# Kernel tuning notes

Measured on AMD Instinct MI355X. Metric: run time of the kernel, lower is better.

Reference implementation:

```python
import jax, jax.numpy as jnp
import numpy as np

NUM_LEVELS = 3      # init: nums_levels
SAMPLE_POINTS = 9   # init: sample_points (S+1 = 10 samples per level)


def _ste_ceil(x):
    # straight-through ceil: forward ceil(x), gradient identity
    return jnp.ceil(x) - jax.lax.stop_gradient(x) + x


def _ste_floor(x):
    return jnp.floor(x) - jax.lax.stop_gradient(x) + x


def _local_cost_volume(cv, cur_disp, radius, sample_nums):
    # cv: [B,D,H,W], cur_disp: [B,1,H,W]
    B, D, H, W = cv.shape
    lower = cur_disp - radius                                   # [B,1,H,W]
    interval = (2.0 * radius) / sample_nums                     # scalar (upper-lower)/S
    steps = jnp.arange(sample_nums + 1, dtype=cv.dtype).reshape(1, -1, 1, 1)
    cand = lower + steps * interval                             # [B,S+1,H,W]
    ceil_c = jnp.clip(_ste_ceil(cand), 0, D - 1)
    floor_c = jnp.clip(_ste_floor(cand), 0, D - 1)
    floor_rate = ceil_c - cand
    ceil_rate = 1.0 - floor_rate
    idx_c = jax.lax.stop_gradient(ceil_c).astype(jnp.int32)
    idx_f = jax.lax.stop_gradient(floor_c).astype(jnp.int32)
    vol_c = jnp.take_along_axis(cv, idx_c, axis=1)              # gather along D
    vol_f = jnp.take_along_axis(cv, idx_f, axis=1)
    return vol_c * ceil_rate + vol_f * floor_rate               # [B,S+1,H,W]


def setup_inputs() -> dict:
    key = jax.random.key(0)
    k1, k2 = jax.random.split(key)
    B, D, H, W = 16, 64, 128, 240
    cost_volume = jax.random.normal(k1, (B, D, H, W), dtype=jnp.float32)
    # current disparity estimate in [0, D-1)
    cur_disp = jax.random.uniform(k2, (B, 1, H, W), dtype=jnp.float32) * (D - 1)
    return {"cost_volume": cost_volume, "radius": 4, "cur_disp": cur_disp}


def reference(cost_volume, radius, cur_disp):
    # Build pyramid by pairwise averaging along the disparity dim
    # (equivalent to the permute + avg_pool1d(2,2) + permute in the original).
    pyramid = [cost_volume]
    cv = cost_volume
    for _ in range(NUM_LEVELS - 1):
        B, D, H, W = cv.shape
        cv = cv.reshape(B, D // 2, 2, H, W).mean(axis=2)
        pyramid.append(cv)
    outs = []
    for i in range(NUM_LEVELS):
        ref_disp = cur_disp / (2.0 ** i)
        outs.append(_local_cost_volume(pyramid[i], ref_disp, float(radius), SAMPLE_POINTS))
    return jnp.concatenate(outs, axis=1)  # [B, NUM_LEVELS*(S+1), H, W]
```

## Files before the change

kernel.cpp:

```cpp
#include <hip/hip_runtime.h>
#include <hip/hip_fp16.h>

#define BB 16
#define DD 64
#define HH 128
#define WW 240
#define HW (HH * WW)
#define NS 10
#define NL 3
#define BLK 256
#define NWORD (DD / 2)
#define GRID 512
#define NTILE (BB * HW / BLK)

__device__ inline unsigned pack2h(float lo, float hi) {
    __half2 h = __floats2half2_rn(lo, hi);
    return *reinterpret_cast<unsigned*>(&h);
}
__device__ inline float2 unpack2h(unsigned u) {
    __half2 h = *reinterpret_cast<__half2*>(&u);
    return __half22float2(h);
}
__device__ inline float exth(unsigned u, int sel) {
    unsigned short us = (unsigned short)(u >> (sel << 4));
    __half_raw hr; hr.x = us;
    return __half2float(*reinterpret_cast<__half*>(&hr));
}

__global__ __launch_bounds__(BLK) void pcv_kernel(
    const float* __restrict__ cv,
    const int* __restrict__ radius_p,
    const float* __restrict__ disp_in,
    float* __restrict__ out)
{
    __shared__ unsigned ldsw[2][NWORD * BLK];
    const int tid = threadIdx.x;
    const int bid = blockIdx.x;
    const int q  = tid & 63;
    const int jb = tid >> 6;

    const float r = (float)(*radius_p);
    const float interval = (float)((2.0 * (double)r) / 9.0);

    const int ntiles = (NTILE - bid + GRID - 1) / GRID;

    float4 rv[16];
    float  dsp;

    {
        const int t = bid;
        const int pb = t * BLK;
        const int b = pb / HW;
        const int pixbase = pb - b * HW;
        const float* src = cv + (size_t)b * DD * HW + pixbase;
        #pragma unroll
        for (int it = 0; it < 8; ++it) {
            const int j = it * 4 + jb;
            rv[2 * it]     = *reinterpret_cast<const float4*>(src + (size_t)(2 * j)     * HW + q * 4);
            rv[2 * it + 1] = *reinterpret_cast<const float4*>(src + (size_t)(2 * j + 1) * HW + q * 4);
        }
        dsp = disp_in[pb + tid];
    }

    int cur = 0;
    for (int k = 0; k < ntiles; ++k) {
        const int t = bid + k * GRID;
        const int pb = t * BLK;
        const int b = pb / HW;
        const int pix = pb - b * HW + tid;

        unsigned* buf = &ldsw[cur][0];
        #pragma unroll
        for (int it = 0; it < 8; ++it) {
            const int j = it * 4 + jb;
            uint4 wv;
            wv.x = pack2h(rv[2 * it].x, rv[2 * it + 1].x);
            wv.y = pack2h(rv[2 * it].y, rv[2 * it + 1].y);
            wv.z = pack2h(rv[2 * it].z, rv[2 * it + 1].z);
            wv.w = pack2h(rv[2 * it].w, rv[2 * it + 1].w);
            *reinterpret_cast<uint4*>(&buf[j * BLK + q * 4]) = wv;
        }
        const float disp = dsp;

        if (k + 1 < ntiles) {
            const int tn = bid + (k + 1) * GRID;
            const int pbn = tn * BLK;
            const int bn = pbn / HW;
            const int pixbase_n = pbn - bn * HW;
            const float* srcn = cv + (size_t)bn * DD * HW + pixbase_n;
            #pragma unroll
            for (int it = 0; it < 8; ++it) {
                const int j = it * 4 + jb;
                rv[2 * it]     = *reinterpret_cast<const float4*>(srcn + (size_t)(2 * j)     * HW + q * 4);
                rv[2 * it + 1] = *reinterpret_cast<const float4*>(srcn + (size_t)(2 * j + 1) * HW + q * 4);
            }
            dsp = disp_in[pbn + tid];
        }

        asm volatile("s_waitcnt lgkmcnt(0)\n\ts_barrier" ::: "memory");

        float* outp = out + (size_t)b * (NL * NS) * HW + pix;
        float rd = disp;
        int Dl = DD;
        #pragma unroll
        for (int lvl = 0; lvl < NL; ++lvl) {
            const float lower = rd - r;
            const float dmax = (float)(Dl - 1);
            #pragma unroll
            for (int s = 0; s < NS; ++s) {
                float cand = lower + (float)s * interval;
                float cc = fminf(fmaxf(ceilf(cand),  0.0f), dmax);
                float fc = fminf(fmaxf(floorf(cand), 0.0f), dmax);
                float fr = cc - cand;
                float cr = 1.0f - fr;
                int ic = (int)cc;
                int fi = (int)fc;
                float vc, vf;
                if (lvl == 0) {
                    unsigned uf = buf[(fi >> 1) * BLK + tid];
                    unsigned uc = buf[(ic >> 1) * BLK + tid];
                    vf = exth(uf, fi & 1);
                    vc = exth(uc, ic & 1);
                } else if (lvl == 1) {
                    float2 a = unpack2h(buf[fi * BLK + tid]);
                    float2 c = unpack2h(buf[ic * BLK + tid]);
                    vf = 0.5f * (a.x + a.y);
                    vc = 0.5f * (c.x + c.y);
                } else {
                    float2 a0 = unpack2h(buf[(2 * fi)     * BLK + tid]);
                    float2 a1 = unpack2h(buf[(2 * fi + 1) * BLK + tid]);
                    float2 c0 = unpack2h(buf[(2 * ic)     * BLK + tid]);
                    float2 c1 = unpack2h(buf[(2 * ic + 1) * BLK + tid]);
                    vf = 0.5f * (0.5f * (a0.x + a0.y) + 0.5f * (a1.x + a1.y));
                    vc = 0.5f * (0.5f * (c0.x + c0.y) + 0.5f * (c1.x + c1.y));
                }
                outp[(size_t)(lvl * NS + s) * HW] = vc * cr + vf * fr;
            }
            rd *= 0.5f;
            Dl >>= 1;
        }
        cur ^= 1;
    }
}

extern "C" void kernel_launch(void* const* d_in, const int* in_sizes, int n_in,
                              void* d_out, int out_size, void* d_ws, size_t ws_size,
                              hipStream_t stream) {
    const float* cv     = (const float*)d_in[0];
    const int*   radius = (const int*)  d_in[1];
    const float* disp   = (const float*)d_in[2];
    float*       out    = (float*)d_out;

    pcv_kernel<<<dim3(GRID), dim3(BLK), 0, stream>>>(cv, radius, disp, out);
}
```

Before: 37.32 us.

## Split pixel tile across two thread halves sharing samples, shrink tile to 128

Halves the pixel tile per block to 128 and has the two halves of the block each compute five of the ten samples per level for the same pixels, instead of one thread doing all ten. This halves per-thread prefetch registers and LDS per block, which allows launch bounds of 4 blocks per CU and a larger grid of 960 with an exact, compile-time iteration count. The cost is more blocks and more tiles, so barrier and prefetch overhead is amortized over less work per tile.

```diff
diff --git a/kernel.cpp b/kernel.cpp
--- a/kernel.cpp
+++ b/kernel.cpp
@@ -9,9 +9,11 @@
 #define NS 10
 #define NL 3
 #define BLK 256
+#define TPIX 128
 #define NWORD (DD / 2)
-#define GRID 512
-#define NTILE (BB * HW / BLK)
+#define NTILE (BB * HW / TPIX)
+#define GRID 960
+#define KITER (NTILE / GRID)
 
 __device__ inline unsigned pack2h(float lo, float hi) {
     __half2 h = __floats2half2_rn(lo, hi);
@@ -27,74 +29,71 @@
     return __half2float(*reinterpret_cast<__half*>(&hr));
 }
 
-__global__ __launch_bounds__(BLK) void pcv_kernel(
+__global__ __launch_bounds__(BLK, 4) void pcv_kernel(
     const float* __restrict__ cv,
     const int* __restrict__ radius_p,
     const float* __restrict__ disp_in,
     float* __restrict__ out)
 {
-    __shared__ unsigned ldsw[2][NWORD * BLK];
+    __shared__ unsigned ldsw[2][NWORD * TPIX];
     const int tid = threadIdx.x;
     const int bid = blockIdx.x;
-    const int q  = tid & 63;
-    const int jb = tid >> 6;
+    const int slot = tid & 31;
+    const int jg   = tid >> 5;
+    const int px   = tid & 127;
+    const int shalf = tid >> 7;
 
     const float r = (float)(*radius_p);
     const float interval = (float)((2.0 * (double)r) / 9.0);
 
-    const int ntiles = (NTILE - bid + GRID - 1) / GRID;
-
-    float4 rv[16];
+    float4 rva[4], rvb[4];
     float  dsp;
 
     {
-        const int t = bid;
-        const int pb = t * BLK;
+        const int pb = bid * TPIX;
         const int b = pb / HW;
         const int pixbase = pb - b * HW;
         const float* src = cv + (size_t)b * DD * HW + pixbase;
         #pragma unroll
-        for (int it = 0; it < 8; ++it) {
-            const int j = it * 4 + jb;
-            rv[2 * it]     = *reinterpret_cast<const float4*>(src + (size_t)(2 * j)     * HW + q * 4);
-            rv[2 * it + 1] = *reinterpret_cast<const float4*>(src + (size_t)(2 * j + 1) * HW + q * 4);
+        for (int it = 0; it < 4; ++it) {
+            const int j = it * 8 + jg;
+            rva[it] = *reinterpret_cast<const float4*>(src + (size_t)(2 * j)     * HW + slot * 4);
+            rvb[it] = *reinterpret_cast<const float4*>(src + (size_t)(2 * j + 1) * HW + slot * 4);
         }
-        dsp = disp_in[pb + tid];
+        dsp = disp_in[pb + px];
     }
 
     int cur = 0;
-    for (int k = 0; k < ntiles; ++k) {
+    for (int k = 0; k < KITER; ++k) {
         const int t = bid + k * GRID;
-        const int pb = t * BLK;
+        const int pb = t * TPIX;
         const int b = pb / HW;
-        const int pix = pb - b * HW + tid;
+        const int pix = pb - b * HW + px;
 
         unsigned* buf = &ldsw[cur][0];
         #pragma unroll
-        for (int it = 0; it < 8; ++it) {
-            const int j = it * 4 + jb;
+        for (int it = 0; it < 4; ++it) {
+            const int j = it * 8 + jg;
             uint4 wv;
-            wv.x = pack2h(rv[2 * it].x, rv[2 * it + 1].x);
-            wv.y = pack2h(rv[2 * it].y, rv[2 * it + 1].y);
-            wv.z = pack2h(rv[2 * it].z, rv[2 * it + 1].z);
-            wv.w = pack2h(rv[2 * it].w, rv[2 * it + 1].w);
-            *reinterpret_cast<uint4*>(&buf[j * BLK + q * 4]) = wv;
+            wv.x = pack2h(rva[it].x, rvb[it].x);
+            wv.y = pack2h(rva[it].y, rvb[it].y);
+            wv.z = pack2h(rva[it].z, rvb[it].z);
+            wv.w = pack2h(rva[it].w, rvb[it].w);
+            *reinterpret_cast<uint4*>(&buf[j * TPIX + slot * 4]) = wv;
         }
         const float disp = dsp;
 
-        if (k + 1 < ntiles) {
-            const int tn = bid + (k + 1) * GRID;
-            const int pbn = tn * BLK;
+        if (k + 1 < KITER) {
+            const int pbn = (t + GRID) * TPIX;
             const int bn = pbn / HW;
-            const int pixbase_n = pbn - bn * HW;
-            const float* srcn = cv + (size_t)bn * DD * HW + pixbase_n;
+            const float* srcn = cv + (size_t)bn * DD * HW + (pbn - bn * HW);
             #pragma unroll
-            for (int it = 0; it < 8; ++it) {
-                const int j = it * 4 + jb;
-                rv[2 * it]     = *reinterpret_cast<const float4*>(srcn + (size_t)(2 * j)     * HW + q * 4);
-                rv[2 * it + 1] = *reinterpret_cast<const float4*>(srcn + (size_t)(2 * j + 1) * HW + q * 4);
+            for (int it = 0; it < 4; ++it) {
+                const int j = it * 8 + jg;
+                rva[it] = *reinterpret_cast<const float4*>(srcn + (size_t)(2 * j)     * HW + slot * 4);
+                rvb[it] = *reinterpret_cast<const float4*>(srcn + (size_t)(2 * j + 1) * HW + slot * 4);
             }
-            dsp = disp_in[pbn + tid];
+            dsp = disp_in[pbn + px];
         }
 
         asm volatile("s_waitcnt lgkmcnt(0)\n\ts_barrier" ::: "memory");
@@ -107,7 +106,8 @@
             const float lower = rd - r;
             const float dmax = (float)(Dl - 1);
             #pragma unroll
-            for (int s = 0; s < NS; ++s) {
+            for (int s5 = 0; s5 < 5; ++s5) {
+                const int s = shalf * 5 + s5;
                 float cand = lower + (float)s * interval;
                 float cc = fminf(fmaxf(ceilf(cand),  0.0f), dmax);
                 float fc = fminf(fmaxf(floorf(cand), 0.0f), dmax);
@@ -117,20 +117,20 @@
                 int fi = (int)fc;
                 float vc, vf;
                 if (lvl == 0) {
-                    unsigned uf = buf[(fi >> 1) * BLK + tid];
-                    unsigned uc = buf[(ic >> 1) * BLK + tid];
+                    unsigned uf = buf[(fi >> 1) * TPIX + px];
+                    unsigned uc = buf[(ic >> 1) * TPIX + px];
                     vf = exth(uf, fi & 1);
                     vc = exth(uc, ic & 1);
                 } else if (lvl == 1) {
-                    float2 a = unpack2h(buf[fi * BLK + tid]);
-                    float2 c = unpack2h(buf[ic * BLK + tid]);
+                    float2 a = unpack2h(buf[fi * TPIX + px]);
+                    float2 c = unpack2h(buf[ic * TPIX + px]);
                     vf = 0.5f * (a.x + a.y);
                     vc = 0.5f * (c.x + c.y);
                 } else {
-                    float2 a0 = unpack2h(buf[(2 * fi)     * BLK + tid]);
-                    float2 a1 = unpack2h(buf[(2 * fi + 1) * BLK + tid]);
-                    float2 c0 = unpack2h(buf[(2 * ic)     * BLK + tid]);
-                    float2 c1 = unpack2h(buf[(2 * ic + 1) * BLK + tid]);
+                    float2 a0 = unpack2h(buf[(2 * fi)     * TPIX + px]);
+                    float2 a1 = unpack2h(buf[(2 * fi + 1) * TPIX + px]);
+                    float2 c0 = unpack2h(buf[(2 * ic)     * TPIX + px]);
+                    float2 c1 = unpack2h(buf[(2 * ic + 1) * TPIX + px]);
                     vf = 0.5f * (0.5f * (a0.x + a0.y) + 0.5f * (a1.x + a1.y));
                     vc = 0.5f * (0.5f * (c0.x + c0.y) + 0.5f * (c1.x + c1.y));
                 }
```

New measurement: 33.64 us. -9.9%, faster.
